# Optimization experiments

Hardware: AMD Instinct MI355X
Metric: run time of the kernel (lower is better)

## Reference

```python
import jax, jax.numpy as jnp
import numpy as np
import math

N = 8192
IN_FEATURES = 512
OUT_FEATURES = 512
BUCKET = 4          # self.bucket -> number of hash buckets
NHASH = 1           # nHashTable hardcoded to 1 in forward
NEG = -9e15         # sentinel used by the original module


def setup_inputs() -> dict:
    key = jax.random.key(0)
    k_in, k_adj, k_rot, k_kw, k_vw = jax.random.split(key, 5)
    inp = jax.random.normal(k_in, (N, IN_FEATURES), dtype=jnp.float32)
    adj = jax.random.randint(k_adj, (N, N), 0, 2, dtype=jnp.int32)
    rotations_rands = jax.random.normal(k_rot, (NHASH, OUT_FEATURES, BUCKET // 2), dtype=jnp.float32)
    # xavier_uniform with gain=1.414 for (in, out) matrices
    limit = 1.414 * math.sqrt(6.0 / (IN_FEATURES + OUT_FEATURES))
    kW = jax.random.uniform(k_kw, (IN_FEATURES, OUT_FEATURES), minval=-limit, maxval=limit, dtype=jnp.float32)
    vW = jax.random.uniform(k_vw, (IN_FEATURES, OUT_FEATURES), minval=-limit, maxval=limit, dtype=jnp.float32)
    return {"input": inp, "adj": adj, "rotations_rands": rotations_rands, "kW": kW, "vW": vW}


def reference(input, adj, rotations_rands, kW, vW):
    kh = input @ kW                      # [N, H]
    vh = input @ vW                      # [N, H]
    H = kh.shape[1]

    # LSH bucketing: rotate keys, argmax over [r, -r] -> bucket id per node
    rv = jnp.einsum('nh,thb->tnb', kh, rotations_rands)   # [1, N, B/2]
    rv = jnp.concatenate([rv, -rv], axis=-1)              # [1, N, B]
    buckets = jnp.argmax(rv, axis=2)[0]                   # [N]

    # Original scatters per-bucket kh@kh.T blocks into a dense NxN matrix
    # initialized at NEG; equivalent to masking full scores by same-bucket.
    same_bucket = buckets[:, None] == buckets[None, :]    # [N, N]
    scores = (kh @ kh.T) / jnp.sqrt(jnp.asarray(H, kh.dtype))
    K = jnp.where(same_bucket, scores, NEG)

    attention = jnp.where(adj > 0, K, NEG)
    attention = jax.nn.softmax(attention, axis=1)
    # dropout is identity in eval mode (reference runs in eval)
    h_prime = attention @ vh                              # [N, H]
    return jax.nn.elu(h_prime)                            # concat=True -> ELU
```

## Files before the change

### kernel.cpp

```cpp
#include <hip/hip_runtime.h>
#include <hip/hip_bf16.h>
#include <math.h>

#define N_NODES 8192
#define FEAT 512
#define NEGV -9e15f
#define VHPT_W 8704

typedef __attribute__((ext_vector_type(8))) short short8;
typedef __attribute__((ext_vector_type(4))) float floatx4;

#define OFF_KH    0UL
#define OFF_VH    16777216UL
#define OFF_KHP   33554432UL
#define OFF_VHPT  42074112UL
#define OFF_MASK  50987008UL
#define OFF_S     59375616UL
#define OFF_PERM  109707264UL
#define OFF_FLAGS 109740032UL
#define OFF_BUCK  109772800UL
#define OFF_META  109805568UL
#define OFF_CMEAN 109806592UL
#define WS_NEEDED 109808640UL
#define CAP_S     25165824L

#define OFF_AHI   (OFF_S)
#define OFF_ALO   (OFF_S + 8388608UL)
#define OFF_WKHI  (OFF_S + 16777216UL)
#define OFF_WKLO  (OFF_S + 17301504UL)
#define OFF_WVHI  (OFF_S + 17825792UL)
#define OFF_WVLO  (OFF_S + 18350080UL)
#define OFF_CW    (OFF_MASK)

static __device__ __forceinline__ unsigned short f2bf_bits(float x) {
  __hip_bfloat16 h = __float2bfloat16(x);
  unsigned short u;
  __builtin_memcpy(&u, &h, 2);
  return u;
}
static __device__ __forceinline__ float bf_bits2f(unsigned short u) {
  __hip_bfloat16 h;
  __builtin_memcpy(&h, &u, 2);
  return __bfloat162float(h);
}

static __device__ __forceinline__ void async_copy16(const void* gptr,
                                                    void* lptr) {
  __builtin_amdgcn_global_load_lds(
      (const __attribute__((address_space(1))) unsigned int*)gptr,
      (__attribute__((address_space(3))) unsigned int*)lptr, 16, 0, 0);
}

__global__ __launch_bounds__(256) void convert_input(
    const float* __restrict__ A, __hip_bfloat16* __restrict__ Ahi,
    __hip_bfloat16* __restrict__ Alo) {
  const long idx = ((long)blockIdx.x * 256 + threadIdx.x) * 4;
  const float4 v = *(const float4*)&A[idx];
  const float vv[4] = {v.x, v.y, v.z, v.w};
  ushort4 hi, lo;
  unsigned short* hp = (unsigned short*)&hi;
  unsigned short* lp = (unsigned short*)&lo;
#pragma unroll
  for (int e = 0; e < 4; e++) {
    unsigned short h = f2bf_bits(vv[e]);
    hp[e] = h;
    lp[e] = f2bf_bits(vv[e] - bf_bits2f(h));
  }
  *(ushort4*)&Ahi[idx] = hi;
  *(ushort4*)&Alo[idx] = lo;
}

__global__ __launch_bounds__(256) void convert_w(
    const float* __restrict__ kW, const float* __restrict__ vW,
    __hip_bfloat16* __restrict__ WkhiT, __hip_bfloat16* __restrict__ WkloT,
    __hip_bfloat16* __restrict__ WvhiT, __hip_bfloat16* __restrict__ WvloT) {
  __shared__ float tile[64][65];
  const int z = blockIdx.z;
  const float* __restrict__ W = z ? vW : kW;
  __hip_bfloat16* __restrict__ HiT = z ? WvhiT : WkhiT;
  __hip_bfloat16* __restrict__ LoT = z ? WvloT : WkloT;
  const int k0 = blockIdx.x * 64, n0 = blockIdx.y * 64;
  const int t = threadIdx.x;
#pragma unroll
  for (int s = 0; s < 16; s++) {
    int idx = t + s * 256;
    int r = idx >> 6, c = idx & 63;
    tile[r][c] = W[(long)(k0 + r) * FEAT + n0 + c];
  }
  __syncthreads();
#pragma unroll
  for (int s = 0; s < 16; s++) {
    int idx = t + s * 256;
    int a = idx >> 6, b = idx & 63;
    float w = tile[b][a];
    unsigned short h = f2bf_bits(w);
    unsigned short l = f2bf_bits(w - bf_bits2f(h));
    __builtin_memcpy(&HiT[(long)(n0 + a) * FEAT + k0 + b], &h, 2);
    __builtin_memcpy(&LoT[(long)(n0 + a) * FEAT + k0 + b], &l, 2);
  }
}

__global__ __launch_bounds__(256) void mfma_dual(
    const __hip_bfloat16* __restrict__ Ahi, const __hip_bfloat16* __restrict__ Alo,
    const __hip_bfloat16* __restrict__ WkhiT, const __hip_bfloat16* __restrict__ WkloT,
    const __hip_bfloat16* __restrict__ WvhiT, const __hip_bfloat16* __restrict__ WvloT,
    float* __restrict__ kh, float* __restrict__ vh) {
  const int z = blockIdx.z;
  const __hip_bfloat16* __restrict__ WhiT = z ? WvhiT : WkhiT;
  const __hip_bfloat16* __restrict__ WloT = z ? WvloT : WkloT;
  float* __restrict__ outp = z ? vh : kh;
  const int ti = blockIdx.x, tj = blockIdx.y;
  __shared__ __align__(16) __hip_bfloat16 Ah[128 * 32];
  __shared__ __align__(16) __hip_bfloat16 Al[128 * 32];
  __shared__ __align__(16) __hip_bfloat16 Wh[128 * 32];
  __shared__ __align__(16) __hip_bfloat16 Wl[128 * 32];
  const int t = threadIdx.x;
  const int lane = t & 63, w = t >> 6;
  const int wm = (w >> 1) * 64, wn = (w & 1) * 64;
  const int quad = lane >> 4, ln = lane & 15;
  const int qr = quad * 8;
  floatx4 acc[4][4];
#pragma unroll
  for (int mi = 0; mi < 4; mi++)
#pragma unroll
    for (int ni = 0; ni < 4; ni++) acc[mi][ni] = (floatx4)0.f;
  for (int k0 = 0; k0 < FEAT; k0 += 32) {
    __syncthreads();
#pragma unroll
    for (int s = 0; s < 2; s++) {
      int c = t + s * 256;
      int row = c >> 2, off8 = (c & 3) * 8;
      int lo = row * 32 + off8;
      async_copy16(&Ahi[(long)(ti * 128 + row) * FEAT + k0 + off8], &Ah[lo]);
      async_copy16(&Alo[(long)(ti * 128 + row) * FEAT + k0 + off8], &Al[lo]);
      async_copy16(&WhiT[(long)(tj * 128 + row) * FEAT + k0 + off8], &Wh[lo]);
      async_copy16(&WloT[(long)(tj * 128 + row) * FEAT + k0 + off8], &Wl[lo]);
    }
    __syncthreads();
    short8 ah[4], al[4], bh[4], bl[4];
#pragma unroll
    for (int mi = 0; mi < 4; mi++) {
      ah[mi] = *(const short8*)&Ah[(wm + mi * 16 + ln) * 32 + qr];
      al[mi] = *(const short8*)&Al[(wm + mi * 16 + ln) * 32 + qr];
    }
#pragma unroll
    for (int ni = 0; ni < 4; ni++) {
      bh[ni] = *(const short8*)&Wh[(wn + ni * 16 + ln) * 32 + qr];
      bl[ni] = *(const short8*)&Wl[(wn + ni * 16 + ln) * 32 + qr];
    }
#pragma unroll
    for (int mi = 0; mi < 4; mi++)
#pragma unroll
      for (int ni = 0; ni < 4; ni++) {
        acc[mi][ni] = __builtin_amdgcn_mfma_f32_16x16x32_bf16(
            ah[mi], bh[ni], acc[mi][ni], 0, 0, 0);
        acc[mi][ni] = __builtin_amdgcn_mfma_f32_16x16x32_bf16(
            ah[mi], bl[ni], acc[mi][ni], 0, 0, 0);
        acc[mi][ni] = __builtin_amdgcn_mfma_f32_16x16x32_bf16(
            al[mi], bh[ni], acc[mi][ni], 0, 0, 0);
      }
  }
#pragma unroll
  for (int mi = 0; mi < 4; mi++)
#pragma unroll
    for (int ni = 0; ni < 4; ni++) {
      int cc = tj * 128 + wn + ni * 16 + ln;
#pragma unroll
      for (int reg = 0; reg < 4; reg++) {
        int r = ti * 128 + wm + mi * 16 + quad * 4 + reg;
        outp[(long)r * FEAT + cc] = acc[mi][ni][reg];
      }
    }
}

__global__ __launch_bounds__(64) void cw_kernel(
    const float* __restrict__ kW, const float* __restrict__ rot,
    double* __restrict__ cw) {
  const int f = blockIdx.x;
  const int lane = threadIdx.x;
  double r0 = 0.0, r1 = 0.0;
  for (int h = lane; h < FEAT; h += 64) {
    double a = (double)kW[(long)f * FEAT + h];
    r0 += a * (double)rot[2 * h];
    r1 += a * (double)rot[2 * h + 1];
  }
#pragma unroll
  for (int off = 32; off > 0; off >>= 1) {
    r0 += __shfl_down(r0, off);
    r1 += __shfl_down(r1, off);
  }
  if (lane == 0) {
    cw[2 * f] = r0;
    cw[2 * f + 1] = r1;
  }
}

__global__ __launch_bounds__(64) void rv_bucket_kernel(
    const float* __restrict__ input, const double* __restrict__ cw,
    int* __restrict__ buckets) {
  const int i = blockIdx.x;
  const int lane = threadIdx.x;
  double r0 = 0.0, r1 = 0.0;
  for (int f = lane; f < FEAT; f += 64) {
    double a = (double)input[(long)i * FEAT + f];
    r0 += a * cw[2 * f];
    r1 += a * cw[2 * f + 1];
  }
#pragma unroll
  for (int off = 32; off > 0; off >>= 1) {
    r0 += __shfl_down(r0, off);
    r1 += __shfl_down(r1, off);
  }
  if (lane == 0) {
    int b = 0;
    double best = r0;
    if (r1 > best)  { best = r1;  b = 1; }
    if (-r0 > best) { best = -r0; b = 2; }
    if (-r1 > best) { best = -r1; b = 3; }
    buckets[i] = b;
  }
}

__global__ __launch_bounds__(256) void sort_kernel(
    const int* __restrict__ buckets, int* __restrict__ perm,
    int* __restrict__ meta, float* __restrict__ cmean) {
  __shared__ int lc[4][256];
  __shared__ int sc[4][256];
  __shared__ int boff_sh[5];
  const int t = threadIdx.x;
  cmean[t] = 0.f;
  cmean[t + 256] = 0.f;
  const int base = t * 32;
  int c0 = 0, c1 = 0, c2 = 0, c3 = 0;
  for (int k = 0; k < 32; k++) {
    int b = buckets[base + k];
    c0 += (b == 0); c1 += (b == 1); c2 += (b == 2); c3 += (b == 3);
  }
  lc[0][t] = c0; lc[1][t] = c1; lc[2][t] = c2; lc[3][t] = c3;
  sc[0][t] = c0; sc[1][t] = c1; sc[2][t] = c2; sc[3][t] = c3;
  __syncthreads();
  for (int off = 1; off < 256; off <<= 1) {
    int a0 = (t >= off) ? sc[0][t - off] : 0;
    int a1 = (t >= off) ? sc[1][t - off] : 0;
    int a2 = (t >= off) ? sc[2][t - off] : 0;
    int a3 = (t >= off) ? sc[3][t - off] : 0;
    __syncthreads();
    sc[0][t] += a0; sc[1][t] += a1; sc[2][t] += a2; sc[3][t] += a3;
    __syncthreads();
  }
  if (t == 0) {
    int boff[5];
    boff[0] = 0;
    for (int b = 0; b < 4; b++) boff[b + 1] = boff[b] + sc[b][255];
    for (int b = 0; b < 5; b++) { meta[b] = boff[b]; boff_sh[b] = boff[b]; }
    long so = 0;
    int po = 0;
    for (int b = 0; b < 4; b++) {
      int tot = boff[b + 1] - boff[b];
      int pad = ((tot + 127) >> 7) << 7;
      meta[5 + b] = pad;
      meta[9 + b] = (int)so;
      meta[14 + b] = po;
      so += (long)pad * pad;
      po += pad;
    }
    meta[13] = (int)so;
    meta[18] = po;
    if (so > CAP_S)
      for (int b = 0; b < 4; b++) meta[5 + b] = 0;
  }
  __syncthreads();
  int s0 = boff_sh[0] + sc[0][t] - lc[0][t];
  int s1 = boff_sh[1] + sc[1][t] - lc[1][t];
  int s2 = boff_sh[2] + sc[2][t] - lc[2][t];
  int s3 = boff_sh[3] + sc[3][t] - lc[3][t];
  for (int k = 0; k < 32; k++) {
    int i = base + k;
    int b = buckets[i];
    int pos = (b == 0) ? s0++ : ((b == 1) ? s1++ : ((b == 2) ? s2++ : s3++));
    perm[pos] = i;
  }
}

__global__ __launch_bounds__(256) void gather_khp_kernel(
    const float* __restrict__ kh, const int* __restrict__ perm,
    __hip_bfloat16* __restrict__ khp) {
  const int g = blockIdx.x;
  const int t = threadIdx.x;
  if (g < N_NODES) {
    const int p = perm[g];
    const float2 v = *(const float2*)&kh[(long)p * FEAT + 2 * t];
    khp[(long)g * FEAT + 2 * t] = __float2bfloat16(v.x);
    khp[(long)g * FEAT + 2 * t + 1] = __float2bfloat16(v.y);
  } else {
    khp[(long)g * FEAT + 2 * t] = __float2bfloat16(0.f);
    khp[(long)g * FEAT + 2 * t + 1] = __float2bfloat16(0.f);
  }
}

__global__ __launch_bounds__(256) void transpose_vhpT_kernel(
    const float* __restrict__ vh, const int* __restrict__ perm,
    const int* __restrict__ meta, __hip_bfloat16* __restrict__ vhpT,
    float* __restrict__ cmean) {
  __shared__ float tile[64][65];
  __shared__ float cred[4][64];
  const int g0 = blockIdx.x * 64;
  const int f0 = blockIdx.y * 64;
  const int t = threadIdx.x;
#pragma unroll
  for (int s = 0; s < 16; s++) {
    int idx = t + s * 256;
    int r = idx >> 6, c = idx & 63;
    int pos = g0 + r;
    int b = (pos >= meta[15]) + (pos >= meta[16]) + (pos >= meta[17]);
    int local = pos - meta[14 + b];
    int n_b = meta[b + 1] - meta[b];
    float v = 0.f;
    if (local < n_b) v = vh[(long)perm[meta[b] + local] * FEAT + f0 + c];
    tile[r][c] = v;
  }
  __syncthreads();
  {
    const int c = t & 63, seg = t >> 6;
    float ps = 0.f;
#pragma unroll
    for (int rr = 0; rr < 16; rr++) ps += tile[seg * 16 + rr][c];
    cred[seg][c] = ps;
  }
  __syncthreads();
  if (t < 64)
    atomicAdd(&cmean[f0 + t],
              cred[0][t] + cred[1][t] + cred[2][t] + cred[3][t]);
#pragma unroll
  for (int s = 0; s < 16; s++) {
    int idx = t + s * 256;
    int fr = idx >> 6, gc = idx & 63;
    vhpT[(long)(f0 + fr) * VHPT_W + g0 + gc] = __float2bfloat16(tile[gc][fr]);
  }
}

__global__ __launch_bounds__(256) void maskpack_kernel(
    const int* __restrict__ adj, const int* __restrict__ perm,
    const int* __restrict__ meta, unsigned long long* __restrict__ maskbits) {
  __shared__ int adj_lds[N_NODES];
  const int g = blockIdx.x;
  const int t = threadIdx.x;
  const int b = (g >= meta[1]) + (g >= meta[2]) + (g >= meta[3]);
  const int boff = meta[b];
  const int n_b = meta[b + 1] - boff;
  const int padded = meta[5 + b];
  const int i = perm[g];
  const int* arow = adj + (long)i * N_NODES;
#pragma unroll
  for (int s = 0; s < 8; s++) {
    int idx = (t + s * 256) * 4;
    *(int4*)&adj_lds[idx] = *(const int4*)&arow[idx];
  }
  __syncthreads();
  const int lane = t & 63, w = t >> 6;
  for (int jj0 = w * 64; jj0 < padded; jj0 += 256) {
    int jj = jj0 + lane;
    int pred = 0;
    if (jj < n_b) pred = adj_lds[perm[boff + jj]] > 0;
    unsigned long long mword = __ballot(pred);
    if (lane == 0) maskbits[(long)g * 128 + (jj0 >> 6)] = mword;
  }
}

__global__ __launch_bounds__(256) void s_gemm(
    const __hip_bfloat16* __restrict__ khp, const int* __restrict__ meta,
    const unsigned long long* __restrict__ maskbits,
    __hip_bfloat16* __restrict__ S) {
  const int b = blockIdx.z;
  const int padded = meta[5 + b];
  const int ti = blockIdx.x, tj = blockIdx.y;
  if (ti * 128 >= padded || tj * 128 >= padded || tj < ti) return;
  const int boff = meta[b];
  const long soff = meta[9 + b];
  __shared__ __align__(16) __hip_bfloat16 smem[128 * 136];
  __hip_bfloat16* As = smem;
  __hip_bfloat16* Bs = smem + 128 * 32;
  const int t = threadIdx.x;
  const int lane = t & 63, w = t >> 6;
  const int wm = (w >> 1) * 64, wn = (w & 1) * 64;
  const int quad = lane >> 4, ln = lane & 15;
  const int qr = quad * 8;
  floatx4 acc[4][4];
#pragma unroll
  for (int mi = 0; mi < 4; mi++)
#pragma unroll
    for (int ni = 0; ni < 4; ni++) acc[mi][ni] = (floatx4)0.f;
  const long a_g0 = boff + ti * 128;
  const long b_g0 = boff + tj * 128;
  for (int k0 = 0; k0 < FEAT; k0 += 32) {
    __syncthreads();
#pragma unroll
    for (int s = 0; s < 2; s++) {
      int c = t + s * 256;
      int row = c >> 2, off8 = (c & 3) * 8;
      int lo = row * 32 + off8;
      async_copy16(&khp[(a_g0 + row) * FEAT + k0 + off8], &As[lo]);
      async_copy16(&khp[(b_g0 + row) * FEAT + k0 + off8], &Bs[lo]);
    }
    __syncthreads();
    short8 af[4], bfr[4];
#pragma unroll
    for (int mi = 0; mi < 4; mi++)
      af[mi] = *(const short8*)&As[(wm + mi * 16 + ln) * 32 + qr];
#pragma unroll
    for (int ni = 0; ni < 4; ni++)
      bfr[ni] = *(const short8*)&Bs[(wn + ni * 16 + ln) * 32 + qr];
#pragma unroll
    for (int mi = 0; mi < 4; mi++)
#pragma unroll
      for (int ni = 0; ni < 4; ni++)
        acc[mi][ni] = __builtin_amdgcn_mfma_f32_16x16x32_bf16(
            af[mi], bfr[ni], acc[mi][ni], 0, 0, 0);
  }
  const float scale = 0.04419417382415922f;
  __syncthreads();
  __hip_bfloat16* Ct = smem;
#pragma unroll
  for (int mi = 0; mi < 4; mi++)
#pragma unroll
    for (int ni = 0; ni < 4; ni++) {
      int col = wn + ni * 16 + ln;
#pragma unroll
      for (int reg = 0; reg < 4; reg++) {
        int row = wm + mi * 16 + quad * 4 + reg;
        Ct[row * 136 + col] = __float2bfloat16(acc[mi][ni][reg] * scale);
      }
    }
  __syncthreads();
  const unsigned short negb = f2bf_bits(NEGV);
#pragma unroll
  for (int i = 0; i < 8; i++) {
    int idx = t + i * 256;
    int rl = idx >> 4, c8 = (idx & 15) * 8;
    int rg = ti * 128 + rl;
    int cg = tj * 128 + c8;
    union { short8 v; unsigned short u[8]; } pk;
    pk.v = *(const short8*)&Ct[rl * 136 + c8];
    unsigned long long wbits = maskbits[(long)(boff + rg) * 128 + (cg >> 6)];
#pragma unroll
    for (int e = 0; e < 8; e++)
      if (!((wbits >> ((cg & 63) + e)) & 1ULL)) pk.u[e] = negb;
    *(short8*)&S[soff + (long)rg * padded + cg] = pk.v;
  }
  if (ti != tj) {
#pragma unroll
    for (int i = 0; i < 8; i++) {
      int idx = t + i * 256;
      int cl = idx >> 4, r8 = (idx & 15) * 8;
      int rg = tj * 128 + cl;
      int cg = ti * 128 + r8;
      union { short8 v; unsigned short u[8]; } pk;
#pragma unroll
      for (int e = 0; e < 8; e++) {
        __hip_bfloat16 hv = Ct[(r8 + e) * 136 + cl];
        __builtin_memcpy(&pk.u[e], &hv, 2);
      }
      unsigned long long wbits = maskbits[(long)(boff + rg) * 128 + (cg >> 6)];
#pragma unroll
      for (int e = 0; e < 8; e++)
        if (!((wbits >> ((cg & 63) + e)) & 1ULL)) pk.u[e] = negb;
      *(short8*)&S[soff + (long)rg * padded + cg] = pk.v;
    }
  }
}

__global__ __launch_bounds__(256) void softmax_kernel(
    __hip_bfloat16* __restrict__ S, const int* __restrict__ meta,
    int* __restrict__ flags) {
  const int g = blockIdx.x;
  const int b = (g >= meta[1]) + (g >= meta[2]) + (g >= meta[3]);
  const int boff = meta[b];
  const int padded = meta[5 + b];
  const long soff = meta[9 + b];
  __hip_bfloat16* row = S + soff + (long)(g - boff) * padded;
  __shared__ float red[256];
  __shared__ float pb[8192];
  const int t = threadIdx.x;
  float m = -INFINITY;
  for (int j0 = t * 8; j0 < padded; j0 += 2048) {
    union { short8 v; unsigned short u[8]; } pk;
    pk.v = *(const short8*)&row[j0];
#pragma unroll
    for (int e = 0; e < 8; e++) {
      float s = bf_bits2f(pk.u[e]);
      pb[j0 + e] = s;
      m = fmaxf(m, s);
    }
  }
  red[t] = m;
  __syncthreads();
#pragma unroll
  for (int o = 128; o > 0; o >>= 1) {
    if (t < o) red[t] = fmaxf(red[t], red[t + o]);
    __syncthreads();
  }
  m = red[0];
  __syncthreads();
  if (m < -8e15f) {
    if (t == 0) flags[g] = 1;
    union { short8 v; unsigned short u[8]; } zz;
#pragma unroll
    for (int e = 0; e < 8; e++) zz.u[e] = 0;
    for (int j0 = t * 8; j0 < padded; j0 += 2048) *(short8*)&row[j0] = zz.v;
    return;
  }
  if (t == 0) flags[g] = 0;
  float sum = 0.f;
  for (int j0 = t * 8; j0 < padded; j0 += 2048) {
#pragma unroll
    for (int e = 0; e < 8; e++) {
      float ex = expf(pb[j0 + e] - m);
      pb[j0 + e] = ex;
      sum += ex;
    }
  }
  red[t] = sum;
  __syncthreads();
#pragma unroll
  for (int o = 128; o > 0; o >>= 1) {
    if (t < o) red[t] += red[t + o];
    __syncthreads();
  }
  const float inv = 1.f / red[0];
  for (int j0 = t * 8; j0 < padded; j0 += 2048) {
    union { short8 v; unsigned short u[8]; } pk;
#pragma unroll
    for (int e = 0; e < 8; e++) pk.u[e] = f2bf_bits(pb[j0 + e] * inv);
    *(short8*)&row[j0] = pk.v;
  }
}

__global__ __launch_bounds__(256) void pv_gemm(
    const __hip_bfloat16* __restrict__ S, const __hip_bfloat16* __restrict__ vhpT,
    const int* __restrict__ meta, const int* __restrict__ perm,
    const int* __restrict__ flags, const float* __restrict__ cmean,
    float* __restrict__ out) {
  const int b = blockIdx.z;
  const int padded = meta[5 + b];
  const int ti = blockIdx.x;
  if (ti * 128 >= padded) return;
  const int boff = meta[b];
  const int n_b = meta[b + 1] - boff;
  const long soff = meta[9 + b];
  const int poff = meta[14 + b];
  const int f0 = blockIdx.y * 64;
  __shared__ __align__(16) __hip_bfloat16 As[128 * 32];
  __shared__ __align__(16) __hip_bfloat16 Bs[64 * 32];
  const int t = threadIdx.x;
  const int lane = t & 63, w = t >> 6;
  const int wm = w * 32;
  const int quad = lane >> 4, ln = lane & 15;
  const int qr = quad * 8;
  floatx4 acc[2][4];
#pragma unroll
  for (int mi = 0; mi < 2; mi++)
#pragma unroll
    for (int ni = 0; ni < 4; ni++) acc[mi][ni] = (floatx4)0.f;
  const long r0 = (long)ti * 128;
  for (int k0 = 0; k0 < padded; k0 += 32) {
    __syncthreads();
#pragma unroll
    for (int s = 0; s < 2; s++) {
      int c = t + s * 256;
      int row = c >> 2, off8 = (c & 3) * 8;
      async_copy16(&S[soff + (r0 + row) * padded + k0 + off8],
                   &As[row * 32 + off8]);
    }
    {
      int row = t >> 2, off8 = (t & 3) * 8;
      async_copy16(&vhpT[(long)(f0 + row) * VHPT_W + poff + k0 + off8],
                   &Bs[row * 32 + off8]);
    }
    __syncthreads();
    short8 af[2], bfr[4];
#pragma unroll
    for (int mi = 0; mi < 2; mi++)
      af[mi] = *(const short8*)&As[(wm + mi * 16 + ln) * 32 + qr];
#pragma unroll
    for (int ni = 0; ni < 4; ni++)
      bfr[ni] = *(const short8*)&Bs[(ni * 16 + ln) * 32 + qr];
#pragma unroll
    for (int mi = 0; mi < 2; mi++)
#pragma unroll
      for (int ni = 0; ni < 4; ni++)
        acc[mi][ni] = __builtin_amdgcn_mfma_f32_16x16x32_bf16(
            af[mi], bfr[ni], acc[mi][ni], 0, 0, 0);
  }
#pragma unroll
  for (int mi = 0; mi < 2; mi++) {
#pragma unroll
    for (int reg = 0; reg < 4; reg++) {
      int r = ti * 128 + wm + mi * 16 + quad * 4 + reg;
      if (r < n_b) {
        int g = boff + r;
        int node = perm[g];
        int fl = flags[g];
#pragma unroll
        for (int ni = 0; ni < 4; ni++) {
          int fc = f0 + ni * 16 + ln;
          float v = fl ? cmean[fc] * (1.f / (float)N_NODES)
                       : acc[mi][ni][reg];
          v = v > 0.f ? v : expm1f(v);
          out[(long)node * FEAT + fc] = v;
        }
      }
    }
  }
}

__global__ __launch_bounds__(256) void gemm_dual(
    const float* __restrict__ A, const float* __restrict__ Wk,
    const float* __restrict__ Wv, float* __restrict__ kh,
    float* __restrict__ vh) {
  __shared__ float As[32][33];
  __shared__ float Bk[32][33];
  __shared__ float Bv[32][33];
  const int tid = threadIdx.x;
  const int row0 = blockIdx.x * 32;
  const int col0 = blockIdx.y * 32;
  const int tx = tid & 15, ty = tid >> 4;
  float ck00 = 0.f, ck01 = 0.f, ck10 = 0.f, ck11 = 0.f;
  float cv00 = 0.f, cv01 = 0.f, cv10 = 0.f, cv11 = 0.f;
  for (int kt = 0; kt < FEAT; kt += 32) {
#pragma unroll
    for (int t = 0; t < 4; t++) {
      int e = tid + t * 256;
      int r = e >> 5, c = e & 31;
      As[r][c] = A[(long)(row0 + r) * FEAT + kt + c];
      Bk[r][c] = Wk[(long)(kt + r) * FEAT + col0 + c];
      Bv[r][c] = Wv[(long)(kt + r) * FEAT + col0 + c];
    }
    __syncthreads();
#pragma unroll
    for (int kk = 0; kk < 32; kk++) {
      float a0 = As[ty * 2][kk], a1 = As[ty * 2 + 1][kk];
      float bk0 = Bk[kk][tx * 2], bk1 = Bk[kk][tx * 2 + 1];
      float bv0 = Bv[kk][tx * 2], bv1 = Bv[kk][tx * 2 + 1];
      ck00 += a0 * bk0; ck01 += a0 * bk1;
      ck10 += a1 * bk0; ck11 += a1 * bk1;
      cv00 += a0 * bv0; cv01 += a0 * bv1;
      cv10 += a1 * bv0; cv11 += a1 * bv1;
    }
    __syncthreads();
  }
  const int r0 = row0 + ty * 2, c0 = col0 + tx * 2;
  kh[(long)r0 * FEAT + c0] = ck00;       kh[(long)r0 * FEAT + c0 + 1] = ck01;
  kh[(long)(r0 + 1) * FEAT + c0] = ck10; kh[(long)(r0 + 1) * FEAT + c0 + 1] = ck11;
  vh[(long)r0 * FEAT + c0] = cv00;       vh[(long)r0 * FEAT + c0 + 1] = cv01;
  vh[(long)(r0 + 1) * FEAT + c0] = cv10; vh[(long)(r0 + 1) * FEAT + c0 + 1] = cv11;
}

__global__ __launch_bounds__(64) void bucket_kernel(
    const float* __restrict__ kh, const float* __restrict__ rot,
    int* __restrict__ buckets) {
  const int i = blockIdx.x;
  const int lane = threadIdx.x;
  double r0 = 0.0, r1 = 0.0;
  for (int h = lane; h < FEAT; h += 64) {
    double a = (double)kh[(long)i * FEAT + h];
    r0 += a * (double)rot[2 * h];
    r1 += a * (double)rot[2 * h + 1];
  }
#pragma unroll
  for (int off = 32; off > 0; off >>= 1) {
    r0 += __shfl_down(r0, off);
    r1 += __shfl_down(r1, off);
  }
  if (lane == 0) {
    int b = 0;
    double best = r0;
    if (r1 > best)  { best = r1;  b = 1; }
    if (-r0 > best) { best = -r0; b = 2; }
    if (-r1 > best) { best = -r1; b = 3; }
    buckets[i] = b;
  }
}

__global__ __launch_bounds__(256) void attn_kernel(
    const float* __restrict__ kh, const float* __restrict__ vh,
    const int* __restrict__ adj, const int* __restrict__ buckets,
    float* __restrict__ out) {
  __shared__ float khi[FEAT];
  __shared__ float pbuf[N_NODES];
  __shared__ unsigned short jlist[N_NODES];
  __shared__ int cnt_sh;
  __shared__ float red[256];
  const int i = blockIdx.x;
  const int tid = threadIdx.x;
  if (tid == 0) cnt_sh = 0;
  for (int k = tid; k < FEAT; k += 256) khi[k] = kh[(long)i * FEAT + k];
  const int mybucket = buckets[i];
  __syncthreads();
  const int* adjrow = adj + (long)i * N_NODES;
  for (int j = tid; j < N_NODES; j += 256) {
    if (adjrow[j] > 0 && buckets[j] == mybucket) {
      int idx = atomicAdd(&cnt_sh, 1);
      jlist[idx] = (unsigned short)j;
    }
  }
  __syncthreads();
  const int cnt = cnt_sh;
  float mloc = -INFINITY;
  for (int idx = tid; idx < cnt; idx += 256) {
    int j = jlist[idx];
    const float4* kj = (const float4*)(kh + (long)j * FEAT);
    const float4* ki = (const float4*)khi;
    float acc = 0.f;
#pragma unroll 8
    for (int k = 0; k < FEAT / 4; k++) {
      float4 a = ki[k];
      float4 b = kj[k];
      acc += a.x * b.x + a.y * b.y + a.z * b.z + a.w * b.w;
    }
    float s = acc * 0.04419417382415922f;
    pbuf[idx] = s;
    mloc = fmaxf(mloc, s);
  }
  red[tid] = mloc;
  __syncthreads();
#pragma unroll
  for (int off = 128; off > 0; off >>= 1) {
    if (tid < off) red[tid] = fmaxf(red[tid], red[tid + off]);
    __syncthreads();
  }
  const float m = red[0];
  __syncthreads();
  float lloc = 0.f;
  for (int idx = tid; idx < cnt; idx += 256) {
    float p = expf(pbuf[idx] - m);
    pbuf[idx] = p;
    lloc += p;
  }
  red[tid] = lloc;
  __syncthreads();
#pragma unroll
  for (int off = 128; off > 0; off >>= 1) {
    if (tid < off) red[tid] += red[tid + off];
    __syncthreads();
  }
  const float l = red[0];
  __syncthreads();
  const int f = 2 * tid;
  float acc0 = 0.f, acc1 = 0.f;
  if (cnt > 0) {
#pragma unroll 4
    for (int idx = 0; idx < cnt; idx++) {
      int j = jlist[idx];
      float p = pbuf[idx];
      float2 v = *(const float2*)(vh + (long)j * FEAT + f);
      acc0 += p * v.x;
      acc1 += p * v.y;
    }
    float invl = 1.f / l;
    acc0 *= invl;
    acc1 *= invl;
  } else {
    for (int j = 0; j < N_NODES; j++) {
      float2 v = *(const float2*)(vh + (long)j * FEAT + f);
      acc0 += v.x;
      acc1 += v.y;
    }
    acc0 *= (1.f / (float)N_NODES);
    acc1 *= (1.f / (float)N_NODES);
  }
  acc0 = acc0 > 0.f ? acc0 : expm1f(acc0);
  acc1 = acc1 > 0.f ? acc1 : expm1f(acc1);
  *(float2*)(out + (long)i * FEAT + f) = make_float2(acc0, acc1);
}

extern "C" void kernel_launch(void* const* d_in, const int* in_sizes, int n_in,
                              void* d_out, int out_size, void* d_ws,
                              size_t ws_size, hipStream_t stream) {
  const float* input = (const float*)d_in[0];
  const int* adj = (const int*)d_in[1];
  const float* rot = (const float*)d_in[2];
  const float* kW = (const float*)d_in[3];
  const float* vW = (const float*)d_in[4];
  float* out = (float*)d_out;

  char* ws = (char*)d_ws;

  if (ws_size >= WS_NEEDED) {
    float* kh = (float*)(ws + OFF_KH);
    float* vh = (float*)(ws + OFF_VH);
    __hip_bfloat16* khp = (__hip_bfloat16*)(ws + OFF_KHP);
    __hip_bfloat16* vhpT = (__hip_bfloat16*)(ws + OFF_VHPT);
    unsigned long long* maskbits = (unsigned long long*)(ws + OFF_MASK);
    __hip_bfloat16* S = (__hip_bfloat16*)(ws + OFF_S);
    int* perm = (int*)(ws + OFF_PERM);
    int* flags = (int*)(ws + OFF_FLAGS);
    int* buckets = (int*)(ws + OFF_BUCK);
    int* meta = (int*)(ws + OFF_META);
    float* cmean = (float*)(ws + OFF_CMEAN);
    __hip_bfloat16* Ahi = (__hip_bfloat16*)(ws + OFF_AHI);
    __hip_bfloat16* Alo = (__hip_bfloat16*)(ws + OFF_ALO);
    __hip_bfloat16* WkhiT = (__hip_bfloat16*)(ws + OFF_WKHI);
    __hip_bfloat16* WkloT = (__hip_bfloat16*)(ws + OFF_WKLO);
    __hip_bfloat16* WvhiT = (__hip_bfloat16*)(ws + OFF_WVHI);
    __hip_bfloat16* WvloT = (__hip_bfloat16*)(ws + OFF_WVLO);
    double* cw = (double*)(ws + OFF_CW);

    convert_input<<<4096, 256, 0, stream>>>(input, Ahi, Alo);
    convert_w<<<dim3(8, 8, 2), 256, 0, stream>>>(kW, vW, WkhiT, WkloT, WvhiT,
                                                 WvloT);
    mfma_dual<<<dim3(64, 4, 2), 256, 0, stream>>>(Ahi, Alo, WkhiT, WkloT,
                                                  WvhiT, WvloT, kh, vh);
    cw_kernel<<<512, 64, 0, stream>>>(kW, rot, cw);
    rv_bucket_kernel<<<N_NODES, 64, 0, stream>>>(input, cw, buckets);
    sort_kernel<<<1, 256, 0, stream>>>(buckets, perm, meta, cmean);
    gather_khp_kernel<<<N_NODES + 128, 256, 0, stream>>>(kh, perm, khp);
    transpose_vhpT_kernel<<<dim3(VHPT_W / 64, FEAT / 64), 256, 0, stream>>>(
        vh, perm, meta, vhpT, cmean);
    maskpack_kernel<<<N_NODES, 256, 0, stream>>>(adj, perm, meta, maskbits);
    s_gemm<<<dim3(64, 64, 4), 256, 0, stream>>>(khp, meta, maskbits, S);
    softmax_kernel<<<N_NODES, 256, 0, stream>>>(S, meta, flags);
    pv_gemm<<<dim3(64, 8, 4), 256, 0, stream>>>(S, vhpT, meta, perm, flags,
                                                cmean, out);
  } else {
    float* kh = (float*)(ws + 0UL);
    float* vh = (float*)(ws + 16777216UL);
    int* buckets = (int*)(ws + 33554432UL);
    dim3 gemm_grid(N_NODES / 32, FEAT / 32);
    gemm_dual<<<gemm_grid, 256, 0, stream>>>(input, kW, vW, kh, vh);
    bucket_kernel<<<N_NODES, 64, 0, stream>>>(kh, rot, buckets);
    attn_kernel<<<N_NODES, 256, 0, stream>>>(kh, vh, adj, buckets, out);
  }
}
```

Measured before the change: 645.6 us.

## Linearize triangular s_gemm grid, double K-step in GEMMs, wave-per-row softmax

The s_gemm grid becomes a linear index over upper-triangular tile pairs, so blocks no longer launch only to exit early. Both s_gemm and pv_gemm now load 64-wide K slices per sync instead of 32, which halves barrier count at the cost of more LDS. The softmax assigns one wavefront per row and reduces with shuffles instead of LDS trees. It re-reads the row from global memory in each pass rather than caching it in a 32KB LDS buffer, trading extra memory reads and exp recomputation for higher occupancy and no block barriers.

```diff
diff --git a/kernel.cpp b/kernel.cpp
--- a/kernel.cpp
+++ b/kernel.cpp
@@ -373,13 +373,18 @@
     __hip_bfloat16* __restrict__ S) {
   const int b = blockIdx.z;
   const int padded = meta[5 + b];
-  const int ti = blockIdx.x, tj = blockIdx.y;
-  if (ti * 128 >= padded || tj * 128 >= padded || tj < ti) return;
+  const int T = padded >> 7;
+  const int pairs = (T * (T + 1)) >> 1;
+  int L = blockIdx.x;
+  if (L >= pairs) return;
+  int ti = 0;
+  while (L >= T - ti) { L -= T - ti; ti++; }
+  const int tj = ti + L;
   const int boff = meta[b];
   const long soff = meta[9 + b];
   __shared__ __align__(16) __hip_bfloat16 smem[128 * 136];
   __hip_bfloat16* As = smem;
-  __hip_bfloat16* Bs = smem + 128 * 32;
+  __hip_bfloat16* Bs = smem + 2 * 128 * 32;
   const int t = threadIdx.x;
   const int lane = t & 63, w = t >> 6;
   const int wm = (w >> 1) * 64, wn = (w & 1) * 64;
@@ -392,30 +397,37 @@
     for (int ni = 0; ni < 4; ni++) acc[mi][ni] = (floatx4)0.f;
   const long a_g0 = boff + ti * 128;
   const long b_g0 = boff + tj * 128;
-  for (int k0 = 0; k0 < FEAT; k0 += 32) {
-    __syncthreads();
-#pragma unroll
-    for (int s = 0; s < 2; s++) {
-      int c = t + s * 256;
-      int row = c >> 2, off8 = (c & 3) * 8;
-      int lo = row * 32 + off8;
-      async_copy16(&khp[(a_g0 + row) * FEAT + k0 + off8], &As[lo]);
-      async_copy16(&khp[(b_g0 + row) * FEAT + k0 + off8], &Bs[lo]);
-    }
-    __syncthreads();
-    short8 af[4], bfr[4];
-#pragma unroll
-    for (int mi = 0; mi < 4; mi++)
-      af[mi] = *(const short8*)&As[(wm + mi * 16 + ln) * 32 + qr];
-#pragma unroll
-    for (int ni = 0; ni < 4; ni++)
-      bfr[ni] = *(const short8*)&Bs[(wn + ni * 16 + ln) * 32 + qr];
-#pragma unroll
-    for (int mi = 0; mi < 4; mi++)
+  for (int k0 = 0; k0 < FEAT; k0 += 64) {
+    __syncthreads();
+#pragma unroll
+    for (int p = 0; p < 2; p++)
+#pragma unroll
+      for (int s = 0; s < 2; s++) {
+        int c = t + s * 256;
+        int row = c >> 2, off8 = (c & 3) * 8;
+        int lo = p * 4096 + row * 32 + off8;
+        async_copy16(&khp[(a_g0 + row) * FEAT + k0 + p * 32 + off8], &As[lo]);
+        async_copy16(&khp[(b_g0 + row) * FEAT + k0 + p * 32 + off8], &Bs[lo]);
+      }
+    __syncthreads();
+#pragma unroll
+    for (int p = 0; p < 2; p++) {
+      short8 af[4], bfr[4];
+#pragma unroll
+      for (int mi = 0; mi < 4; mi++)
+        af[mi] =
+            *(const short8*)&As[p * 4096 + (wm + mi * 16 + ln) * 32 + qr];
 #pragma unroll
       for (int ni = 0; ni < 4; ni++)
-        acc[mi][ni] = __builtin_amdgcn_mfma_f32_16x16x32_bf16(
-            af[mi], bfr[ni], acc[mi][ni], 0, 0, 0);
+        bfr[ni] =
+            *(const short8*)&Bs[p * 4096 + (wn + ni * 16 + ln) * 32 + qr];
+#pragma unroll
+      for (int mi = 0; mi < 4; mi++)
+#pragma unroll
+        for (int ni = 0; ni < 4; ni++)
+          acc[mi][ni] = __builtin_amdgcn_mfma_f32_16x16x32_bf16(
+              af[mi], bfr[ni], acc[mi][ni], 0, 0, 0);
+    }
   }
   const float scale = 0.04419417382415922f;
   __syncthreads();
@@ -472,65 +484,47 @@
 __global__ __launch_bounds__(256) void softmax_kernel(
     __hip_bfloat16* __restrict__ S, const int* __restrict__ meta,
     int* __restrict__ flags) {
-  const int g = blockIdx.x;
+  const int g = blockIdx.x * 4 + (threadIdx.x >> 6);
+  const int lane = threadIdx.x & 63;
   const int b = (g >= meta[1]) + (g >= meta[2]) + (g >= meta[3]);
   const int boff = meta[b];
   const int padded = meta[5 + b];
   const long soff = meta[9 + b];
   __hip_bfloat16* row = S + soff + (long)(g - boff) * padded;
-  __shared__ float red[256];
-  __shared__ float pb[8192];
-  const int t = threadIdx.x;
   float m = -INFINITY;
-  for (int j0 = t * 8; j0 < padded; j0 += 2048) {
+  for (int j0 = lane * 8; j0 < padded; j0 += 512) {
     union { short8 v; unsigned short u[8]; } pk;
     pk.v = *(const short8*)&row[j0];
 #pragma unroll
-    for (int e = 0; e < 8; e++) {
-      float s = bf_bits2f(pk.u[e]);
-      pb[j0 + e] = s;
-      m = fmaxf(m, s);
-    }
-  }
-  red[t] = m;
-  __syncthreads();
-#pragma unroll
-  for (int o = 128; o > 0; o >>= 1) {
-    if (t < o) red[t] = fmaxf(red[t], red[t + o]);
-    __syncthreads();
-  }
-  m = red[0];
-  __syncthreads();
+    for (int e = 0; e < 8; e++) m = fmaxf(m, bf_bits2f(pk.u[e]));
+  }
+#pragma unroll
+  for (int off = 32; off > 0; off >>= 1) m = fmaxf(m, __shfl_xor(m, off));
   if (m < -8e15f) {
-    if (t == 0) flags[g] = 1;
+    if (lane == 0) flags[g] = 1;
     union { short8 v; unsigned short u[8]; } zz;
 #pragma unroll
     for (int e = 0; e < 8; e++) zz.u[e] = 0;
-    for (int j0 = t * 8; j0 < padded; j0 += 2048) *(short8*)&row[j0] = zz.v;
+    for (int j0 = lane * 8; j0 < padded; j0 += 512) *(short8*)&row[j0] = zz.v;
     return;
   }
-  if (t == 0) flags[g] = 0;
+  if (lane == 0) flags[g] = 0;
   float sum = 0.f;
-  for (int j0 = t * 8; j0 < padded; j0 += 2048) {
-#pragma unroll
-    for (int e = 0; e < 8; e++) {
-      float ex = expf(pb[j0 + e] - m);
-      pb[j0 + e] = ex;
-      sum += ex;
-    }
-  }
-  red[t] = sum;
-  __syncthreads();
-#pragma unroll
-  for (int o = 128; o > 0; o >>= 1) {
-    if (t < o) red[t] += red[t + o];
-    __syncthreads();
-  }
-  const float inv = 1.f / red[0];
-  for (int j0 = t * 8; j0 < padded; j0 += 2048) {
+  for (int j0 = lane * 8; j0 < padded; j0 += 512) {
     union { short8 v; unsigned short u[8]; } pk;
-#pragma unroll
-    for (int e = 0; e < 8; e++) pk.u[e] = f2bf_bits(pb[j0 + e] * inv);
+    pk.v = *(const short8*)&row[j0];
+#pragma unroll
+    for (int e = 0; e < 8; e++) sum += expf(bf_bits2f(pk.u[e]) - m);
+  }
+#pragma unroll
+  for (int off = 32; off > 0; off >>= 1) sum += __shfl_xor(sum, off);
+  const float inv = 1.f / sum;
+  for (int j0 = lane * 8; j0 < padded; j0 += 512) {
+    union { short8 v; unsigned short u[8]; } pk;
+    pk.v = *(const short8*)&row[j0];
+#pragma unroll
+    for (int e = 0; e < 8; e++)
+      pk.u[e] = f2bf_bits(expf(bf_bits2f(pk.u[e]) - m) * inv);
     *(short8*)&row[j0] = pk.v;
   }
 }
@@ -549,8 +543,8 @@
   const long soff = meta[9 + b];
   const int poff = meta[14 + b];
   const int f0 = blockIdx.y * 64;
-  __shared__ __align__(16) __hip_bfloat16 As[128 * 32];
-  __shared__ __align__(16) __hip_bfloat16 Bs[64 * 32];
+  __shared__ __align__(16) __hip_bfloat16 As[2 * 128 * 32];
+  __shared__ __align__(16) __hip_bfloat16 Bs[2 * 64 * 32];
   const int t = threadIdx.x;
   const int lane = t & 63, w = t >> 6;
   const int wm = w * 32;
@@ -562,34 +556,42 @@
 #pragma unroll
     for (int ni = 0; ni < 4; ni++) acc[mi][ni] = (floatx4)0.f;
   const long r0 = (long)ti * 128;
-  for (int k0 = 0; k0 < padded; k0 += 32) {
-    __syncthreads();
-#pragma unroll
-    for (int s = 0; s < 2; s++) {
-      int c = t + s * 256;
-      int row = c >> 2, off8 = (c & 3) * 8;
-      async_copy16(&S[soff + (r0 + row) * padded + k0 + off8],
-                   &As[row * 32 + off8]);
-    }
-    {
-      int row = t >> 2, off8 = (t & 3) * 8;
-      async_copy16(&vhpT[(long)(f0 + row) * VHPT_W + poff + k0 + off8],
-                   &Bs[row * 32 + off8]);
-    }
-    __syncthreads();
-    short8 af[2], bfr[4];
-#pragma unroll
-    for (int mi = 0; mi < 2; mi++)
-      af[mi] = *(const short8*)&As[(wm + mi * 16 + ln) * 32 + qr];
-#pragma unroll
-    for (int ni = 0; ni < 4; ni++)
-      bfr[ni] = *(const short8*)&Bs[(ni * 16 + ln) * 32 + qr];
-#pragma unroll
-    for (int mi = 0; mi < 2; mi++)
+  for (int k0 = 0; k0 < padded; k0 += 64) {
+    __syncthreads();
+#pragma unroll
+    for (int p = 0; p < 2; p++) {
+#pragma unroll
+      for (int s = 0; s < 2; s++) {
+        int c = t + s * 256;
+        int row = c >> 2, off8 = (c & 3) * 8;
+        async_copy16(&S[soff + (r0 + row) * padded + k0 + p * 32 + off8],
+                     &As[p * 4096 + row * 32 + off8]);
+      }
+      {
+        int row = t >> 2, off8 = (t & 3) * 8;
+        async_copy16(
+            &vhpT[(long)(f0 + row) * VHPT_W + poff + k0 + p * 32 + off8],
+            &Bs[p * 2048 + row * 32 + off8]);
+      }
+    }
+    __syncthreads();
+#pragma unroll
+    for (int p = 0; p < 2; p++) {
+      short8 af[2], bfr[4];
+#pragma unroll
+      for (int mi = 0; mi < 2; mi++)
+        af[mi] =
+            *(const short8*)&As[p * 4096 + (wm + mi * 16 + ln) * 32 + qr];
 #pragma unroll
       for (int ni = 0; ni < 4; ni++)
-        acc[mi][ni] = __builtin_amdgcn_mfma_f32_16x16x32_bf16(
-            af[mi], bfr[ni], acc[mi][ni], 0, 0, 0);
+        bfr[ni] = *(const short8*)&Bs[p * 2048 + (ni * 16 + ln) * 32 + qr];
+#pragma unroll
+      for (int mi = 0; mi < 2; mi++)
+#pragma unroll
+        for (int ni = 0; ni < 4; ni++)
+          acc[mi][ni] = __builtin_amdgcn_mfma_f32_16x16x32_bf16(
+              af[mi], bfr[ni], acc[mi][ni], 0, 0, 0);
+    }
   }
 #pragma unroll
   for (int mi = 0; mi < 2; mi++) {
@@ -817,8 +819,8 @@
     transpose_vhpT_kernel<<<dim3(VHPT_W / 64, FEAT / 64), 256, 0, stream>>>(
         vh, perm, meta, vhpT, cmean);
     maskpack_kernel<<<N_NODES, 256, 0, stream>>>(adj, perm, meta, maskbits);
-    s_gemm<<<dim3(64, 64, 4), 256, 0, stream>>>(khp, meta, maskbits, S);
-    softmax_kernel<<<N_NODES, 256, 0, stream>>>(S, meta, flags);
+    s_gemm<<<dim3(2080, 1, 4), 256, 0, stream>>>(khp, meta, maskbits, S);
+    softmax_kernel<<<N_NODES / 4, 256, 0, stream>>>(S, meta, flags);
     pv_gemm<<<dim3(64, 8, 4), 256, 0, stream>>>(S, vhpT, meta, perm, flags,
                                                 cmean, out);
   } else {
```

Result: faster. 588.7 us, median of 2 (-8.8%).
